# Kernel optimization log

Hardware: AMD Instinct MI355X
Metric: run time of the kernel (lower is better)

## Reference

```python
import math
import jax, jax.numpy as jnp
import numpy as np

HEADS = 4
BOTTLENECK = 8

def setup_inputs() -> dict:
    key = jax.random.key(0)
    ks = jax.random.split(key, 12)
    B, N, H, k = 8, 10000, 512, BOTTLENECK
    hd = H // HEADS
    s = 1.0 / math.sqrt(H)
    return {
        "x": jax.random.normal(ks[0], (B, N, H), dtype=jnp.float32),
        "Wq": jax.random.uniform(ks[1], (H, H), jnp.float32, -s, s),
        "bq": jnp.zeros((H,), jnp.float32),
        "Wk": jax.random.uniform(ks[2], (H, H), jnp.float32, -s, s),
        "bk": jnp.zeros((H,), jnp.float32),
        "Wv": jax.random.uniform(ks[3], (H, H), jnp.float32, -s, s),
        "bv": jnp.zeros((H,), jnp.float32),
        "E": jax.random.normal(ks[4], (HEADS, N, k), jnp.float32) / math.sqrt(k),
        "Fp": jax.random.normal(ks[5], (HEADS, N, k), jnp.float32) / math.sqrt(k),
        "gbu": jax.random.normal(ks[6], (HEADS, k, k), jnp.float32) * 0.1,
        "gbv": jax.random.normal(ks[7], (HEADS, k, k), jnp.float32) * 0.1,
        "Wo": jax.random.uniform(ks[8], (H, H), jnp.float32, -s, s),
        "bo": jnp.zeros((H,), jnp.float32),
        "log_reg": jnp.asarray(math.log(1e-5), jnp.float32),
    }

def reference(x, Wq, bq, Wk, bk, Wv, bv, E, Fp, gbu, gbv, Wo, bo, log_reg):
    B, N, H = x.shape
    hd = H // HEADS
    def split_heads(t):
        return t.reshape(B, N, HEADS, hd).transpose(0, 2, 1, 3)  # [B,h,N,hd]
    q = split_heads(x @ Wq.T + bq)
    k = split_heads(x @ Wk.T + bk)
    v = split_heads(x @ Wv.T + bv)
    # Faithful to torch einsum 'hik,bhnd->bhkd' (i and n summed independently)
    k_proj = jnp.einsum('hik,bhnd->bhkd', E, k)   # [B,h,k,hd]
    v_proj = jnp.einsum('hik,bhnd->bhkd', Fp, v)  # [B,h,k,hd]
    scores = jnp.einsum('bhnd,bhkd->bhnk', q, k_proj) / math.sqrt(hd)
    graph_bias = gbu @ gbv                                  # [h,k,k]
    bias_diag = jnp.diagonal(graph_bias, axis1=1, axis2=2)  # [h,k]
    scores = scores + bias_diag[None, :, None, :]
    attn = jax.nn.softmax(scores, axis=-1)
    out = jnp.einsum('bhnk,bhkd->bhnd', attn, v_proj)
    out = out.transpose(0, 2, 1, 3).reshape(B, N, H)
    out = out @ Wo.T + bo
    reg = jnp.exp(log_reg) * (jnp.mean(jnp.abs(attn)) + jnp.mean(jnp.abs(graph_bias)) * 0.1)
    return out, reg
```

## Files before the change

### kernel.cpp

```cpp
#include <hip/hip_runtime.h>
#include <math.h>

#define HEADS 4
#define KB 8
#define Bsz 8
#define Nn 10000
#define Hh 512
#define HD 128
#define NPART 128

#define KSUM_OFF 4096
#define VSUM_OFF 8192
#define WQE_OFF  12288
#define WOE_OFF  28672
#define ESUM_OFF 45056
#define FSUM_OFF 45088
#define BQ_OFF   45120
#define BD_OFF   45152
#define XPART_OFF 45184
#define EFPART_OFF (XPART_OFF + NPART * Bsz * Hh)
#define WS_NEED   (EFPART_OFF + 512)

typedef float f32x4_t __attribute__((ext_vector_type(4)));

__global__ __launch_bounds__(256) void k_part(const float* __restrict__ x,
                                              const float* __restrict__ E,
                                              const float* __restrict__ Fp,
                                              float* __restrict__ xpart,
                                              float* __restrict__ efpart) {
    int blk = blockIdx.x;
    int t = threadIdx.x;
    if (blk < NPART * Bsz) {
        int p = blk >> 3, b = blk & 7;
        const int CH = (Nn + NPART - 1) / NPART;
        int n0 = p * CH, n1 = min(n0 + CH, Nn);
        int c = t * 2;
        float a0 = 0.f, a1 = 0.f;
        const float* base = x + (size_t)b * Nn * Hh + c;
#pragma unroll 8
        for (int n = n0; n < n1; ++n) {
            float2 v = *(const float2*)(base + (size_t)n * Hh);
            a0 += v.x; a1 += v.y;
        }
        float* o = xpart + (size_t)(p * Bsz + b) * Hh;
        o[c] = a0; o[c + 1] = a1;
    } else {
        int idx = blk - NPART * Bsz;
        int src = idx >> 5, h = (idx >> 3) & 3, ch = idx & 7;
        const float* S = src ? Fp : E;
        const int CHE = Nn / 8;
        int n0 = ch * CHE, n1 = n0 + CHE;
        int kk = t & 7, part = t >> 3;
        float acc = 0.f;
        const float* base = S + (size_t)h * Nn * KB;
#pragma unroll 4
        for (int n = n0 + part; n < n1; n += 32) acc += base[n * KB + kk];
        __shared__ float sd[256];
        sd[t] = acc;
        __syncthreads();
        for (int s = 128; s >= 8; s >>= 1) {
            if (t < s) sd[t] += sd[t + s];
            __syncthreads();
        }
        if (t < 8) efpart[idx * 8 + t] = sd[t];
    }
}

__global__ __launch_bounds__(256) void k_reduce(const float* __restrict__ xpart,
                                                const float* __restrict__ efpart,
                                                float* __restrict__ xs,
                                                float* __restrict__ esum,
                                                float* __restrict__ fsum) {
    int blk = blockIdx.x, t = threadIdx.x;
    if (blk < 16) {
        int o = blk * 256 + t;
        float a = 0.f;
#pragma unroll 8
        for (int p = 0; p < NPART; ++p) a += xpart[(size_t)p * (Bsz * Hh) + o];
        xs[o] = a;
    } else if (t < 64) {
        int src = t >> 5, rem = t & 31;
        float a = 0.f;
#pragma unroll
        for (int ch = 0; ch < 8; ++ch)
            a += efpart[((src * 4 + (rem >> 3)) * 8 + ch) * 8 + (rem & 7)];
        if (src == 0) esum[rem] = a; else fsum[rem] = a;
    }
}

__global__ __launch_bounds__(256) void k_gemv(const float* __restrict__ Wk,
                                              const float* __restrict__ bk,
                                              const float* __restrict__ Wv,
                                              const float* __restrict__ bv,
                                              const float* __restrict__ xs,
                                              float* __restrict__ ksum,
                                              float* __restrict__ vsum) {
    int m = blockIdx.x;
    int rg = blockIdx.y;
    const float* W = m ? Wv : Wk;
    const float* bias = m ? bv : bk;
    float* outp = m ? vsum : ksum;
    int t = threadIdx.x;
    int wid = t >> 6, lane = t & 63;
    bool hi32 = (lane & 32) != 0;
    bool hi16 = (lane & 16) != 0;
    bool hi8  = (lane & 8) != 0;

    float4 x0[Bsz], x1[Bsz];
#pragma unroll
    for (int b = 0; b < Bsz; ++b) {
        x0[b] = *(const float4*)(xs + b * Hh + lane * 4);
        x1[b] = *(const float4*)(xs + b * Hh + 256 + lane * 4);
    }
#pragma unroll
    for (int i = 0; i < 4; ++i) {
        int r = rg * 16 + wid + 4 * i;
        float4 wa = *(const float4*)(W + (size_t)r * Hh + lane * 4);
        float4 wb = *(const float4*)(W + (size_t)r * Hh + 256 + lane * 4);
        float p[Bsz];
#pragma unroll
        for (int b = 0; b < Bsz; ++b) {
            p[b] = wa.x * x0[b].x + wa.y * x0[b].y + wa.z * x0[b].z + wa.w * x0[b].w +
                   wb.x * x1[b].x + wb.y * x1[b].y + wb.z * x1[b].z + wb.w * x1[b].w;
        }
        float a, bb;
        a = hi32 ? p[4] : p[0]; bb = hi32 ? p[0] : p[4]; float q0 = a + __shfl_xor(bb, 32, 64);
        a = hi32 ? p[5] : p[1]; bb = hi32 ? p[1] : p[5]; float q1 = a + __shfl_xor(bb, 32, 64);
        a = hi32 ? p[6] : p[2]; bb = hi32 ? p[2] : p[6]; float q2 = a + __shfl_xor(bb, 32, 64);
        a = hi32 ? p[7] : p[3]; bb = hi32 ? p[3] : p[7]; float q3 = a + __shfl_xor(bb, 32, 64);
        a = hi16 ? q2 : q0; bb = hi16 ? q0 : q2; float r0 = a + __shfl_xor(bb, 16, 64);
        a = hi16 ? q3 : q1; bb = hi16 ? q1 : q3; float r1 = a + __shfl_xor(bb, 16, 64);
        a = hi8 ? r1 : r0; bb = hi8 ? r0 : r1; float s = a + __shfl_xor(bb, 8, 64);
        s += __shfl_xor(s, 4, 64);
        s += __shfl_xor(s, 2, 64);
        s += __shfl_xor(s, 1, 64);
        if ((lane & 7) == 0) {
            int b = lane >> 3;
            outp[b * Hh + r] = s + (float)Nn * bias[r];
        }
    }
}

__global__ __launch_bounds__(256) void k_eff2(const float* __restrict__ Wq,
                                              const float* __restrict__ Wo,
                                              const float* __restrict__ ksum,
                                              const float* __restrict__ vsum,
                                              float* __restrict__ wqe,
                                              float* __restrict__ woe,
                                              const float* __restrict__ bq,
                                              const float* __restrict__ gbu,
                                              const float* __restrict__ gbv,
                                              const float* __restrict__ log_reg,
                                              float* __restrict__ bias_q,
                                              float* __restrict__ bias_diag,
                                              float* __restrict__ reg_out) {
    int blk = blockIdx.x;
    int t = threadIdx.x;
    __shared__ float sL[256];
    if (blk < 64) {
        int b = blk >> 3, rem = blk & 7, h = rem >> 1, m = rem & 1;
        const float* s = (m ? vsum : ksum) + b * Hh + h * HD;
        float* out = (m ? woe : wqe) + (size_t)(b * HEADS + h) * Hh;
        if (t < HD) sL[t] = s[t];
        __syncthreads();
        float a0 = 0.f, a1 = 0.f;
        if (m == 0) {
            const float* Wb = Wq + (size_t)h * HD * Hh;
#pragma unroll 4
            for (int d = 0; d < HD; ++d) {
                float sv = sL[d];
                a0 += Wb[(size_t)d * Hh + t] * sv;
                a1 += Wb[(size_t)d * Hh + t + 256] * sv;
            }
        } else {
            const float* W0 = Wo + (size_t)t * Hh + h * HD;
            const float* W1 = Wo + (size_t)(t + 256) * Hh + h * HD;
            for (int d = 0; d < HD; d += 4) {
                a0 += W0[d] * sL[d] + W0[d + 1] * sL[d + 1] + W0[d + 2] * sL[d + 2] + W0[d + 3] * sL[d + 3];
                a1 += W1[d] * sL[d] + W1[d + 1] * sL[d + 1] + W1[d + 2] * sL[d + 2] + W1[d + 3] * sL[d + 3];
            }
        }
        out[t] = a0;
        out[t + 256] = a1;
    } else {
        int h = t >> 6, i = (t >> 3) & 7, j = t & 7;
        float gb = 0.f;
#pragma unroll
        for (int l = 0; l < 8; ++l) gb += gbu[h * 64 + i * 8 + l] * gbv[h * 64 + l * 8 + j];
        if (i == j) bias_diag[h * 8 + i] = gb;
        sL[t] = fabsf(gb);
        __syncthreads();
        for (int s = 128; s >= 1; s >>= 1) {
            if (t < s) sL[t] += sL[t + s];
            __syncthreads();
        }
        if (t == 0) {
            float gbmean = sL[0] / 256.f;
            reg_out[0] = expf(log_reg[0]) * (0.125f + gbmean * 0.1f);
        }
        if (t < 32) {
            int b = t >> 2, hh = t & 3;
            float a = 0.f;
            for (int d = 0; d < HD; ++d) a += bq[hh * HD + d] * ksum[b * Hh + hh * HD + d];
            bias_q[t] = a;
        }
    }
}

__global__ __launch_bounds__(256) void k_main(const float* __restrict__ x,
                                              const float* __restrict__ bo,
                                              const float* __restrict__ wqe,
                                              const float* __restrict__ woe,
                                              const float* __restrict__ esum,
                                              const float* __restrict__ fsum,
                                              const float* __restrict__ bias_q,
                                              const float* __restrict__ bias_diag,
                                              float* __restrict__ out) {
    int b = blockIdx.y;
    int t = threadIdx.x;
    int wid = t >> 6, lane = t & 63;

    const float* wqe_b = wqe + (size_t)b * HEADS * Hh;
    const float* woe_b = woe + (size_t)b * HEADS * Hh;
    float4 wqa[HEADS], wqb[HEADS], woa[HEADS], wob[HEADS];
#pragma unroll
    for (int h = 0; h < HEADS; ++h) {
        wqa[h] = *(const float4*)(wqe_b + h * Hh + lane * 4);
        wqb[h] = *(const float4*)(wqe_b + h * Hh + 256 + lane * 4);
        woa[h] = *(const float4*)(woe_b + h * Hh + lane * 4);
        wob[h] = *(const float4*)(woe_b + h * Hh + 256 + lane * 4);
    }
    float4 boa = *(const float4*)(bo + lane * 4);
    float4 bob = *(const float4*)(bo + 256 + lane * 4);

    int q = lane >> 4;
    int hq = (q == 0) ? 0 : (q == 1) ? 2 : (q == 2) ? 1 : 3;
    int kk = lane & 7;
    float eV = esum[hq * KB + kk];
    float fV = fsum[hq * KB + kk];
    float bdV = bias_diag[hq * KB + kk];
    float bqV = bias_q[b * HEADS + hq];

    const float inv_sqrt_hd = 0.08838834764831843f;
    bool hi32 = (lane & 32) != 0;
    bool hi16 = (lane & 16) != 0;

    int n = blockIdx.x * 4 + wid;
    for (int j = 0; j < 10; ++j, n += 1000) {
        const float* xr = x + ((size_t)b * Nn + n) * Hh;
        float4 xa = *(const float4*)(xr + lane * 4);
        float4 xb = *(const float4*)(xr + 256 + lane * 4);
        float p[HEADS];
#pragma unroll
        for (int h = 0; h < HEADS; ++h) {
            p[h] = xa.x * wqa[h].x + xa.y * wqa[h].y + xa.z * wqa[h].z + xa.w * wqa[h].w +
                   xb.x * wqb[h].x + xb.y * wqb[h].y + xb.z * wqb[h].z + xb.w * wqb[h].w;
        }
        float A  = hi32 ? p[1] : p[0];
        float Bv = hi32 ? p[0] : p[1];
        A += __shfl_xor(Bv, 32, 64);
        float C  = hi32 ? p[3] : p[2];
        float D  = hi32 ? p[2] : p[3];
        C += __shfl_xor(D, 32, 64);
        float Ev = hi16 ? C : A;
        float Fv = hi16 ? A : C;
        Ev += __shfl_xor(Fv, 16, 64);
        Ev += __shfl_xor(Ev, 1, 64);
        Ev += __shfl_xor(Ev, 2, 64);
        Ev += __shfl_xor(Ev, 4, 64);
        Ev += __shfl_xor(Ev, 8, 64);

        float sq = (Ev + bqV) * inv_sqrt_hd;
        float sc = eV * sq + bdV;
        float m = sc;
        m = fmaxf(m, __shfl_xor(m, 1, 64));
        m = fmaxf(m, __shfl_xor(m, 2, 64));
        m = fmaxf(m, __shfl_xor(m, 4, 64));
        float e = __expf(sc - m);
        float se = e, sw = e * fV;
        se += __shfl_xor(se, 1, 64); sw += __shfl_xor(sw, 1, 64);
        se += __shfl_xor(se, 2, 64); sw += __shfl_xor(sw, 2, 64);
        se += __shfl_xor(se, 4, 64); sw += __shfl_xor(sw, 4, 64);
        float wv = __fdividef(sw, se);
        float w0 = __shfl(wv, 0, 64);
        float w2 = __shfl(wv, 16, 64);
        float w1 = __shfl(wv, 32, 64);
        float w3 = __shfl(wv, 48, 64);

        float4 oa = boa, ob = bob;
        oa.x += w0 * woa[0].x + w1 * woa[1].x + w2 * woa[2].x + w3 * woa[3].x;
        oa.y += w0 * woa[0].y + w1 * woa[1].y + w2 * woa[2].y + w3 * woa[3].y;
        oa.z += w0 * woa[0].z + w1 * woa[1].z + w2 * woa[2].z + w3 * woa[3].z;
        oa.w += w0 * woa[0].w + w1 * woa[1].w + w2 * woa[2].w + w3 * woa[3].w;
        ob.x += w0 * wob[0].x + w1 * wob[1].x + w2 * wob[2].x + w3 * wob[3].x;
        ob.y += w0 * wob[0].y + w1 * wob[1].y + w2 * wob[2].y + w3 * wob[3].y;
        ob.z += w0 * wob[0].z + w1 * wob[1].z + w2 * wob[2].z + w3 * wob[3].z;
        ob.w += w0 * wob[0].w + w1 * wob[1].w + w2 * wob[2].w + w3 * wob[3].w;

        float* orow = out + ((size_t)b * Nn + n) * Hh;
        union { float4 s; f32x4_t v; } ua, ub;
        ua.s = oa; ub.s = ob;
        __builtin_nontemporal_store(ua.v, (f32x4_t*)(orow + lane * 4));
        __builtin_nontemporal_store(ub.v, (f32x4_t*)(orow + 256 + lane * 4));
    }
}

extern "C" void kernel_launch(void* const* d_in, const int* in_sizes, int n_in,
                              void* d_out, int out_size, void* d_ws, size_t ws_size,
                              hipStream_t stream) {
    const float* x       = (const float*)d_in[0];
    const float* Wq      = (const float*)d_in[1];
    const float* bq      = (const float*)d_in[2];
    const float* Wk      = (const float*)d_in[3];
    const float* bk      = (const float*)d_in[4];
    const float* Wv      = (const float*)d_in[5];
    const float* bv      = (const float*)d_in[6];
    const float* E       = (const float*)d_in[7];
    const float* Fp      = (const float*)d_in[8];
    const float* gbu     = (const float*)d_in[9];
    const float* gbv     = (const float*)d_in[10];
    const float* Wo      = (const float*)d_in[11];
    const float* bo      = (const float*)d_in[12];
    const float* log_reg = (const float*)d_in[13];

    float* out = (float*)d_out;
    float* ws = (float*)d_ws;
    float* xs   = ws;
    float* ksum = ws + KSUM_OFF;
    float* vsum = ws + VSUM_OFF;
    float* wqe  = ws + WQE_OFF;
    float* woe  = ws + WOE_OFF;
    float* esum = ws + ESUM_OFF;
    float* fsum = ws + FSUM_OFF;
    float* bias_q = ws + BQ_OFF;
    float* bias_diag = ws + BD_OFF;
    float* reg_out = out + (size_t)Bsz * Nn * Hh;

    float* xpart;
    float* efpart;
    if (ws_size >= (size_t)WS_NEED * sizeof(float)) {
        xpart  = ws + XPART_OFF;
        efpart = ws + EFPART_OFF;
    } else {
        xpart  = out;
        efpart = out + (size_t)NPART * Bsz * Hh;
    }

    k_part<<<NPART * Bsz + 64, 256, 0, stream>>>(x, E, Fp, xpart, efpart);
    k_reduce<<<17, 256, 0, stream>>>(xpart, efpart, xs, esum, fsum);
    k_gemv<<<dim3(2, 32), 256, 0, stream>>>(Wk, bk, Wv, bv, xs, ksum, vsum);
    k_eff2<<<65, 256, 0, stream>>>(Wq, Wo, ksum, vsum, wqe, woe,
                                   bq, gbu, gbv, log_reg, bias_q, bias_diag, reg_out);
    k_main<<<dim3(250, Bsz), 256, 0, stream>>>(x, bo, wqe, woe, esum, fsum, bias_q, bias_diag, out);
}
```

Measured before the change: 359.4 us.

## Fuse reduce, gemv and weight-fold kernels into one mid kernel; vectorize partial sums

Merges the partial-sum reduction, the K/V GEMV and the effective-weight computation into a single 65-block kernel. Each block recomputes its own batch's reduced x and the 128 K or V sums it needs into shared memory, which removes two launches and the global round-trips. The partial-sum kernel now uses float4 loads, splits rows across two thread halves and combines them in shared memory. The cost is redundant work: each reduction over partials is repeated per head and matrix, and the GEMV runs on only 64 blocks.

```diff
diff --git a/kernel.cpp b/kernel.cpp
--- a/kernel.cpp
+++ b/kernel.cpp
@@ -30,20 +30,27 @@
                                               float* __restrict__ efpart) {
     int blk = blockIdx.x;
     int t = threadIdx.x;
+    __shared__ float4 sd4[256];
     if (blk < NPART * Bsz) {
         int p = blk >> 3, b = blk & 7;
         const int CH = (Nn + NPART - 1) / NPART;
         int n0 = p * CH, n1 = min(n0 + CH, Nn);
-        int c = t * 2;
-        float a0 = 0.f, a1 = 0.f;
+        int half = t >> 7;
+        int c = (t & 127) * 4;
+        float4 acc = {0.f, 0.f, 0.f, 0.f};
         const float* base = x + (size_t)b * Nn * Hh + c;
-#pragma unroll 8
-        for (int n = n0; n < n1; ++n) {
-            float2 v = *(const float2*)(base + (size_t)n * Hh);
-            a0 += v.x; a1 += v.y;
-        }
-        float* o = xpart + (size_t)(p * Bsz + b) * Hh;
-        o[c] = a0; o[c + 1] = a1;
+#pragma unroll 4
+        for (int n = n0 + half; n < n1; n += 2) {
+            float4 v = *(const float4*)(base + (size_t)n * Hh);
+            acc.x += v.x; acc.y += v.y; acc.z += v.z; acc.w += v.w;
+        }
+        sd4[t] = acc;
+        __syncthreads();
+        if (t < 128) {
+            float4 o = sd4[t], q = sd4[t + 128];
+            o.x += q.x; o.y += q.y; o.z += q.z; o.w += q.w;
+            *(float4*)(xpart + (size_t)(p * Bsz + b) * Hh + t * 4) = o;
+        }
     } else {
         int idx = blk - NPART * Bsz;
         int src = idx >> 5, h = (idx >> 3) & 3, ch = idx & 7;
@@ -55,7 +62,7 @@
         const float* base = S + (size_t)h * Nn * KB;
 #pragma unroll 4
         for (int n = n0 + part; n < n1; n += 32) acc += base[n * KB + kk];
-        __shared__ float sd[256];
+        float* sd = (float*)sd4;
         sd[t] = acc;
         __syncthreads();
         for (int s = 128; s >= 8; s >>= 1) {
@@ -66,123 +73,101 @@
     }
 }
 
-__global__ __launch_bounds__(256) void k_reduce(const float* __restrict__ xpart,
-                                                const float* __restrict__ efpart,
-                                                float* __restrict__ xs,
-                                                float* __restrict__ esum,
-                                                float* __restrict__ fsum) {
-    int blk = blockIdx.x, t = threadIdx.x;
-    if (blk < 16) {
-        int o = blk * 256 + t;
-        float a = 0.f;
-#pragma unroll 8
-        for (int p = 0; p < NPART; ++p) a += xpart[(size_t)p * (Bsz * Hh) + o];
-        xs[o] = a;
-    } else if (t < 64) {
-        int src = t >> 5, rem = t & 31;
-        float a = 0.f;
-#pragma unroll
-        for (int ch = 0; ch < 8; ++ch)
-            a += efpart[((src * 4 + (rem >> 3)) * 8 + ch) * 8 + (rem & 7)];
-        if (src == 0) esum[rem] = a; else fsum[rem] = a;
-    }
-}
-
-__global__ __launch_bounds__(256) void k_gemv(const float* __restrict__ Wk,
-                                              const float* __restrict__ bk,
-                                              const float* __restrict__ Wv,
-                                              const float* __restrict__ bv,
-                                              const float* __restrict__ xs,
-                                              float* __restrict__ ksum,
-                                              float* __restrict__ vsum) {
-    int m = blockIdx.x;
-    int rg = blockIdx.y;
-    const float* W = m ? Wv : Wk;
-    const float* bias = m ? bv : bk;
-    float* outp = m ? vsum : ksum;
-    int t = threadIdx.x;
-    int wid = t >> 6, lane = t & 63;
-    bool hi32 = (lane & 32) != 0;
-    bool hi16 = (lane & 16) != 0;
-    bool hi8  = (lane & 8) != 0;
-
-    float4 x0[Bsz], x1[Bsz];
-#pragma unroll
-    for (int b = 0; b < Bsz; ++b) {
-        x0[b] = *(const float4*)(xs + b * Hh + lane * 4);
-        x1[b] = *(const float4*)(xs + b * Hh + 256 + lane * 4);
-    }
-#pragma unroll
-    for (int i = 0; i < 4; ++i) {
-        int r = rg * 16 + wid + 4 * i;
-        float4 wa = *(const float4*)(W + (size_t)r * Hh + lane * 4);
-        float4 wb = *(const float4*)(W + (size_t)r * Hh + 256 + lane * 4);
-        float p[Bsz];
-#pragma unroll
-        for (int b = 0; b < Bsz; ++b) {
-            p[b] = wa.x * x0[b].x + wa.y * x0[b].y + wa.z * x0[b].z + wa.w * x0[b].w +
-                   wb.x * x1[b].x + wb.y * x1[b].y + wb.z * x1[b].z + wb.w * x1[b].w;
-        }
-        float a, bb;
-        a = hi32 ? p[4] : p[0]; bb = hi32 ? p[0] : p[4]; float q0 = a + __shfl_xor(bb, 32, 64);
-        a = hi32 ? p[5] : p[1]; bb = hi32 ? p[1] : p[5]; float q1 = a + __shfl_xor(bb, 32, 64);
-        a = hi32 ? p[6] : p[2]; bb = hi32 ? p[2] : p[6]; float q2 = a + __shfl_xor(bb, 32, 64);
-        a = hi32 ? p[7] : p[3]; bb = hi32 ? p[3] : p[7]; float q3 = a + __shfl_xor(bb, 32, 64);
-        a = hi16 ? q2 : q0; bb = hi16 ? q0 : q2; float r0 = a + __shfl_xor(bb, 16, 64);
-        a = hi16 ? q3 : q1; bb = hi16 ? q1 : q3; float r1 = a + __shfl_xor(bb, 16, 64);
-        a = hi8 ? r1 : r0; bb = hi8 ? r0 : r1; float s = a + __shfl_xor(bb, 8, 64);
-        s += __shfl_xor(s, 4, 64);
-        s += __shfl_xor(s, 2, 64);
-        s += __shfl_xor(s, 1, 64);
-        if ((lane & 7) == 0) {
-            int b = lane >> 3;
-            outp[b * Hh + r] = s + (float)Nn * bias[r];
-        }
-    }
-}
-
-__global__ __launch_bounds__(256) void k_eff2(const float* __restrict__ Wq,
-                                              const float* __restrict__ Wo,
-                                              const float* __restrict__ ksum,
-                                              const float* __restrict__ vsum,
-                                              float* __restrict__ wqe,
-                                              float* __restrict__ woe,
-                                              const float* __restrict__ bq,
-                                              const float* __restrict__ gbu,
-                                              const float* __restrict__ gbv,
-                                              const float* __restrict__ log_reg,
-                                              float* __restrict__ bias_q,
-                                              float* __restrict__ bias_diag,
-                                              float* __restrict__ reg_out) {
+__global__ __launch_bounds__(256) void k_mid(const float* __restrict__ xpart,
+                                             const float* __restrict__ efpart,
+                                             const float* __restrict__ Wq,
+                                             const float* __restrict__ Wk,
+                                             const float* __restrict__ Wv,
+                                             const float* __restrict__ Wo,
+                                             const float* __restrict__ bq,
+                                             const float* __restrict__ bk,
+                                             const float* __restrict__ bv,
+                                             const float* __restrict__ gbu,
+                                             const float* __restrict__ gbv,
+                                             const float* __restrict__ log_reg,
+                                             float* __restrict__ wqe,
+                                             float* __restrict__ woe,
+                                             float* __restrict__ esum,
+                                             float* __restrict__ fsum,
+                                             float* __restrict__ bias_q,
+                                             float* __restrict__ bias_diag,
+                                             float* __restrict__ reg_out) {
     int blk = blockIdx.x;
     int t = threadIdx.x;
+    __shared__ float xsL[Hh];
+    __shared__ float sumL[HD];
     __shared__ float sL[256];
     if (blk < 64) {
         int b = blk >> 3, rem = blk & 7, h = rem >> 1, m = rem & 1;
-        const float* s = (m ? vsum : ksum) + b * Hh + h * HD;
-        float* out = (m ? woe : wqe) + (size_t)(b * HEADS + h) * Hh;
-        if (t < HD) sL[t] = s[t];
-        __syncthreads();
-        float a0 = 0.f, a1 = 0.f;
+        {
+            float a0 = 0.f, a1 = 0.f;
+            const float* xp = xpart + (size_t)b * Hh;
+#pragma unroll 8
+            for (int p = 0; p < NPART; ++p) {
+                const float* row = xp + (size_t)p * (Bsz * Hh);
+                a0 += row[t]; a1 += row[t + 256];
+            }
+            xsL[t] = a0; xsL[t + 256] = a1;
+        }
+        __syncthreads();
+        {
+            const float* W = m ? Wv : Wk;
+            const float* bias = m ? bv : bk;
+            int wid = t >> 6, lane = t & 63;
+            float4 xa = *(const float4*)(&xsL[lane * 4]);
+            float4 xb = *(const float4*)(&xsL[256 + lane * 4]);
+            for (int i = 0; i < 32; ++i) {
+                int r = wid * 32 + i;
+                const float* wrow = W + (size_t)(h * HD + r) * Hh;
+                float4 wa = *(const float4*)(wrow + lane * 4);
+                float4 wb = *(const float4*)(wrow + 256 + lane * 4);
+                float pd = wa.x * xa.x + wa.y * xa.y + wa.z * xa.z + wa.w * xa.w +
+                           wb.x * xb.x + wb.y * xb.y + wb.z * xb.z + wb.w * xb.w;
+#pragma unroll
+                for (int off = 32; off >= 1; off >>= 1) pd += __shfl_xor(pd, off, 64);
+                if (lane == 0) sumL[r] = pd + (float)Nn * bias[h * HD + r];
+            }
+        }
+        __syncthreads();
         if (m == 0) {
+            float* outp = wqe + (size_t)(b * HEADS + h) * Hh;
             const float* Wb = Wq + (size_t)h * HD * Hh;
+            float a0 = 0.f, a1 = 0.f;
 #pragma unroll 4
             for (int d = 0; d < HD; ++d) {
-                float sv = sL[d];
+                float sv = sumL[d];
                 a0 += Wb[(size_t)d * Hh + t] * sv;
                 a1 += Wb[(size_t)d * Hh + t + 256] * sv;
             }
+            outp[t] = a0;
+            outp[t + 256] = a1;
+            if (t < 64) {
+                float a = bq[h * HD + t] * sumL[t] + bq[h * HD + 64 + t] * sumL[64 + t];
+#pragma unroll
+                for (int off = 32; off >= 1; off >>= 1) a += __shfl_xor(a, off, 64);
+                if (t == 0) bias_q[b * HEADS + h] = a;
+            }
         } else {
+            float* outp = woe + (size_t)(b * HEADS + h) * Hh;
             const float* W0 = Wo + (size_t)t * Hh + h * HD;
             const float* W1 = Wo + (size_t)(t + 256) * Hh + h * HD;
+            float a0 = 0.f, a1 = 0.f;
             for (int d = 0; d < HD; d += 4) {
-                a0 += W0[d] * sL[d] + W0[d + 1] * sL[d + 1] + W0[d + 2] * sL[d + 2] + W0[d + 3] * sL[d + 3];
-                a1 += W1[d] * sL[d] + W1[d + 1] * sL[d + 1] + W1[d + 2] * sL[d + 2] + W1[d + 3] * sL[d + 3];
-            }
-        }
-        out[t] = a0;
-        out[t + 256] = a1;
+                a0 += W0[d] * sumL[d] + W0[d + 1] * sumL[d + 1] + W0[d + 2] * sumL[d + 2] + W0[d + 3] * sumL[d + 3];
+                a1 += W1[d] * sumL[d] + W1[d + 1] * sumL[d + 1] + W1[d + 2] * sumL[d + 2] + W1[d + 3] * sumL[d + 3];
+            }
+            outp[t] = a0;
+            outp[t + 256] = a1;
+        }
     } else {
+        if (t < 64) {
+            int src = t >> 5, rem = t & 31;
+            float a = 0.f;
+#pragma unroll
+            for (int ch = 0; ch < 8; ++ch)
+                a += efpart[((src * 4 + (rem >> 3)) * 8 + ch) * 8 + (rem & 7)];
+            if (src == 0) esum[rem] = a; else fsum[rem] = a;
+        }
         int h = t >> 6, i = (t >> 3) & 7, j = t & 7;
         float gb = 0.f;
 #pragma unroll
@@ -197,12 +182,6 @@
         if (t == 0) {
             float gbmean = sL[0] / 256.f;
             reg_out[0] = expf(log_reg[0]) * (0.125f + gbmean * 0.1f);
-        }
-        if (t < 32) {
-            int b = t >> 2, hh = t & 3;
-            float a = 0.f;
-            for (int d = 0; d < HD; ++d) a += bq[hh * HD + d] * ksum[b * Hh + hh * HD + d];
-            bias_q[t] = a;
         }
     }
 }
@@ -325,9 +304,6 @@
 
     float* out = (float*)d_out;
     float* ws = (float*)d_ws;
-    float* xs   = ws;
-    float* ksum = ws + KSUM_OFF;
-    float* vsum = ws + VSUM_OFF;
     float* wqe  = ws + WQE_OFF;
     float* woe  = ws + WOE_OFF;
     float* esum = ws + ESUM_OFF;
@@ -347,9 +323,8 @@
     }
 
     k_part<<<NPART * Bsz + 64, 256, 0, stream>>>(x, E, Fp, xpart, efpart);
-    k_reduce<<<17, 256, 0, stream>>>(xpart, efpart, xs, esum, fsum);
-    k_gemv<<<dim3(2, 32), 256, 0, stream>>>(Wk, bk, Wv, bv, xs, ksum, vsum);
-    k_eff2<<<65, 256, 0, stream>>>(Wq, Wo, ksum, vsum, wqe, woe,
-                                   bq, gbu, gbv, log_reg, bias_q, bias_diag, reg_out);
+    k_mid<<<65, 256, 0, stream>>>(xpart, efpart, Wq, Wk, Wv, Wo, bq, bk, bv,
+                                  gbu, gbv, log_reg, wqe, woe, esum, fsum,
+                                  bias_q, bias_diag, reg_out);
     k_main<<<dim3(250, Bsz), 256, 0, stream>>>(x, bo, wqe, woe, esum, fsum, bias_q, bias_diag, out);
 }
```

After: 374.2 us. 4.1% more time.
